# Kernel tuning notes

Hardware: AMD Instinct MI355X
Metric: run time of the kernel (lower is better)

The kernel has to match this reference:

```python
import jax, jax.numpy as jnp
import numpy as np

B, S, D = 2, 2048, 1024
H, HD = 16, 64  # H*HD == D (required by proj layer)
SCALE = D ** -0.5  # NOTE: original scales by full input dim (x.shape[-1]), not head dim


def setup_inputs() -> dict:
    key = jax.random.key(0)
    ks = jax.random.split(key, 7)
    std = D ** -0.5
    x = jax.random.normal(ks[0], (B, S, D), dtype=jnp.float32)
    # per-head projection weights, stacked: [H, D, HD] so x @ Wq[h] == Linear(D->HD)
    Wq = jax.random.normal(ks[1], (H, D, HD), dtype=jnp.float32) * std
    Wk = jax.random.normal(ks[2], (H, D, HD), dtype=jnp.float32) * std
    Wv = jax.random.normal(ks[3], (H, D, HD), dtype=jnp.float32) * std
    # output projection Linear(D, D) with bias
    Wp = jax.random.normal(ks[4], (D, D), dtype=jnp.float32) * std
    bp = jax.random.normal(ks[5], (D,), dtype=jnp.float32) * 0.01
    return {"x": x, "Wq": Wq, "Wk": Wk, "Wv": Wv, "Wp": Wp, "bp": bp}


def reference(x, Wq, Wk, Wv, Wp, bp):
    # All heads see the full x (atsp=False path). Dropout in eval mode (identity).
    q = jnp.einsum('bsd,hde->bhse', x, Wq)  # [B,H,S,HD]
    k = jnp.einsum('bsd,hde->bhse', x, Wk)
    v = jnp.einsum('bsd,hde->bhse', x, Wv)
    scores = jnp.einsum('bhse,bhte->bhst', q, k) * SCALE  # [B,H,S,S]
    causal = jnp.tril(jnp.ones((S, S), dtype=bool))
    scores = jnp.where(causal, scores, -jnp.inf)
    attn = jax.nn.softmax(scores, axis=-1)
    out = jnp.einsum('bhst,bhte->bhse', attn, v)          # [B,H,S,HD]
    # concat heads along last dim in head order: [B,S,H*HD]
    out = out.transpose(0, 2, 1, 3).reshape(B, S, H * HD)
    return out @ Wp.T + bp
```

## Files before the change

### kernel.cpp

```cpp
#include <hip/hip_runtime.h>

typedef __bf16 bf16x8 __attribute__((ext_vector_type(8)));
typedef __bf16 bf16x4 __attribute__((ext_vector_type(4)));
typedef float f32x4 __attribute__((ext_vector_type(4)));
typedef unsigned short u16;
typedef unsigned int u32;

static constexpr int kS = 2048, kD = 1024, kHD = 64;
static constexpr float kQScale = 0.03125f * 1.44269504f;

__device__ __forceinline__ u16 f2bf(float f) {
  union { float f; u32 u; } v; v.f = f;
  u32 r = v.u + 0x7FFFu + ((v.u >> 16) & 1u);
  return (u16)(r >> 16);
}
__device__ __forceinline__ float bf2f(u16 u) {
  union { u32 u; float f; } v; v.u = ((u32)u) << 16;
  return v.f;
}
__device__ __forceinline__ u32 pk2(float a, float b) {
  return (u32)f2bf(a) | ((u32)f2bf(b) << 16);
}
__device__ __forceinline__ f32x4 mfma16(bf16x8 a, bf16x8 b, f32x4 c) {
  return __builtin_amdgcn_mfma_f32_16x16x32_bf16(a, b, c, 0, 0, 0);
}
__device__ __forceinline__ void gld16(u16* lds, const u16* g) {
  __builtin_amdgcn_global_load_lds(
      (const __attribute__((address_space(1))) u32*)g,
      (__attribute__((address_space(3))) u32*)lds, 16, 0, 0);
}

__device__ __forceinline__ bool probe_f32(const u16* __restrict__ xr) {
  int ex = (xr[threadIdx.x] >> 7) & 0xFF;
  int n = __syncthreads_count(ex >= 134);
  return n > 8;
}

union Pack8 { u16 u[8]; uint4 v; };

__global__ void cast_all_kernel(const void* Wq, const void* Wk, const void* Wv,
                                const void* Wp, const void* x,
                                u16* __restrict__ Wt, u16* __restrict__ Wpb,
                                u16* __restrict__ xb) {
  bool f32m = probe_f32((const u16*)x);
  int bid = blockIdx.x;
  int t = threadIdx.x;
  __shared__ float Ts[64][65];
  if (bid < 768) {
    int u = bid >> 4;
    int d0 = (bid & 15) * 64;
    int w = u >> 4, h = u & 15;
    const void* srcv = (w == 0) ? Wq : (w == 1) ? Wk : Wv;
    const float* sf = (const float*)srcv + (size_t)h * kD * kHD;
    const u16*   sb = (const u16*)srcv + (size_t)h * kD * kHD;
    int row = t >> 4;
    int c4 = (t & 15) * 4;
    for (int rr = 0; rr < 64; rr += 16) {
      int r = rr + row;
      if (f32m) {
        float4 v = *(const float4*)&sf[(size_t)(d0 + r) * kHD + c4];
        Ts[r][c4 + 0] = v.x; Ts[r][c4 + 1] = v.y; Ts[r][c4 + 2] = v.z; Ts[r][c4 + 3] = v.w;
      } else {
        const u16* p = &sb[(size_t)(d0 + r) * kHD + c4];
        Ts[r][c4 + 0] = bf2f(p[0]); Ts[r][c4 + 1] = bf2f(p[1]);
        Ts[r][c4 + 2] = bf2f(p[2]); Ts[r][c4 + 3] = bf2f(p[3]);
      }
    }
    __syncthreads();
    for (int rr = 0; rr < 64; rr += 16) {
      int e = rr + row;
      uint2 pk;
      pk.x = pk2(Ts[c4 + 0][e], Ts[c4 + 1][e]);
      pk.y = pk2(Ts[c4 + 2][e], Ts[c4 + 3][e]);
      *(uint2*)&Wt[(size_t)u * (kHD * kD) + (size_t)e * kD + d0 + c4] = pk;
    }
  } else if (bid < 1792) {
    if (!f32m) return;
    int i = ((bid - 768) * 256 + t) * 4;
    float4 v = *(const float4*)((const float*)Wp + i);
    uint2 pk; pk.x = pk2(v.x, v.y); pk.y = pk2(v.z, v.w);
    *(uint2*)&Wpb[i] = pk;
  } else {
    if (!f32m) return;
    size_t i = ((size_t)(bid - 1792) * 256 + t) * 8;
    const float* xf = (const float*)x;
    float4 a = *(const float4*)&xf[i];
    float4 b = *(const float4*)&xf[i + 4];
    Pack8 pk;
    pk.u[0] = f2bf(a.x); pk.u[1] = f2bf(a.y); pk.u[2] = f2bf(a.z); pk.u[3] = f2bf(a.w);
    pk.u[4] = f2bf(b.x); pk.u[5] = f2bf(b.y); pk.u[6] = f2bf(b.z); pk.u[7] = f2bf(b.w);
    *(uint4*)&xb[i] = pk.v;
  }
}

__global__ __launch_bounds__(256) void qkv_gemm_kernel(const u16* __restrict__ xb,
    const u16* __restrict__ Wt, u16* __restrict__ Q, u16* __restrict__ K,
    u16* __restrict__ Vt, const void* __restrict__ x) {
  bool f32m = probe_f32((const u16*)x);
  const u16* xsrc = f32m ? xb : (const u16*)x;
  int m0 = blockIdx.x * 128;
  int n0 = blockIdx.y * 128;
  int w = (int)(blockIdx.y >> 3);
  const u16 *Ap, *Bp; int a0, b0;
  if (w == 2) { Ap = xsrc; a0 = m0; Bp = Wt; b0 = n0; }
  else        { Ap = Wt; a0 = n0; Bp = xsrc; b0 = m0; }
  int t = threadIdx.x;
  int wv = t >> 6, l = t & 63;
  int fr = l & 15, fq = l >> 4;
  int wI = (wv >> 1) * 64, wJ = (wv & 1) * 64;
  __shared__ __align__(16) u16 As[128][64];
  __shared__ __align__(16) u16 Bs[128][64];
  int srow = l >> 3;
  int scol = (((l & 7) ^ srow)) * 8;
  int dcol = (l & 7) * 8;
  int sw = fr & 7;
  f32x4 acc[4][4];
#pragma unroll
  for (int ii = 0; ii < 4; ++ii)
#pragma unroll
    for (int jj = 0; jj < 4; ++jj)
      for (int i = 0; i < 4; ++i) acc[ii][jj][i] = 0.f;

  for (int kb = 0; kb < kD / 64; ++kb) {
    int k0 = kb * 64;
    __syncthreads();
#pragma unroll
    for (int j = 0; j < 4; ++j) {
      int row = (wv * 4 + j) * 8 + srow;
      gld16(&As[row][dcol], &Ap[(size_t)(a0 + row) * kD + k0 + scol]);
      gld16(&Bs[row][dcol], &Bp[(size_t)(b0 + row) * kD + k0 + scol]);
    }
    __syncthreads();
    bf16x8 af[4][2], bg[4][2];
#pragma unroll
    for (int ii = 0; ii < 4; ++ii) {
      af[ii][0] = *(const bf16x8*)&As[wI + ii * 16 + fr][((0 + fq) ^ sw) * 8];
      af[ii][1] = *(const bf16x8*)&As[wI + ii * 16 + fr][((4 + fq) ^ sw) * 8];
    }
#pragma unroll
    for (int jj = 0; jj < 4; ++jj) {
      bg[jj][0] = *(const bf16x8*)&Bs[wJ + jj * 16 + fr][((0 + fq) ^ sw) * 8];
      bg[jj][1] = *(const bf16x8*)&Bs[wJ + jj * 16 + fr][((4 + fq) ^ sw) * 8];
    }
#pragma unroll
    for (int ii = 0; ii < 4; ++ii)
#pragma unroll
      for (int jj = 0; jj < 4; ++jj) {
        acc[ii][jj] = mfma16(af[ii][0], bg[jj][0], acc[ii][jj]);
        acc[ii][jj] = mfma16(af[ii][1], bg[jj][1], acc[ii][jj]);
      }
  }

  if (w == 2) {
    int uh = wv & 1;
    int u = 2 * blockIdx.y + uh;
    int h = u & 15;
#pragma unroll
    for (int jj = 0; jj < 4; ++jj) {
      int e = jj * 16 + fr;
#pragma unroll
      for (int ii = 0; ii < 4; ++ii) {
        int m = m0 + wI + ii * 16 + fq * 4;
        int b = m >> 11, s0 = m & 2047;
        int bh = b * 16 + h;
        *(bf16x4*)&Vt[((size_t)bh * kHD + e) * kS + s0] =
            __builtin_convertvector(acc[ii][jj], bf16x4);
      }
    }
  } else {
    int uh = wv >> 1;
    int u = 2 * blockIdx.y + uh;
    int h = u & 15;
    bool isQ = (w == 0);
    u16* dst = isQ ? Q : K;
#pragma unroll
    for (int jj = 0; jj < 4; ++jj) {
      int m = m0 + wJ + jj * 16 + fr;
      int b = m >> 11, s = m & 2047;
      int bh = b * 16 + h;
      size_t rowb = ((size_t)bh * kS + s) * kHD;
#pragma unroll
      for (int ii = 0; ii < 4; ++ii) {
        int e0 = ii * 16 + fq * 4;
        f32x4 v = acc[ii][jj];
        if (isQ) v *= kQScale;
        *(bf16x4*)&dst[rowb + e0] = __builtin_convertvector(v, bf16x4);
      }
    }
  }
}

__global__ __launch_bounds__(256) void attn_kernel(const u16* __restrict__ Q,
    const u16* __restrict__ K, const u16* __restrict__ Vt, u16* __restrict__ cat) {
  int qb = 31 - (int)(blockIdx.x >> 5);
  int bh = (int)(blockIdx.x & 31);
  int q0 = qb * 64;
  int t = threadIdx.x;
  int wv = t >> 6, l = t & 63;
  int fr = l & 15, fq = l >> 4;
  __shared__ __align__(16) u16 Ks[2][64][64];
  __shared__ __align__(16) u16 Vs[2][64][64];
  __shared__ __align__(16) u16 Ps[4][16][64];
  const u16* Qb = Q + (size_t)bh * kS * kHD;
  const u16* Kb = K + (size_t)bh * kS * kHD;
  const u16* Vb = Vt + (size_t)bh * kHD * kS;

  int qrow = q0 + wv * 16 + fr;
  bf16x8 qf0 = *(const bf16x8*)&Qb[(size_t)qrow * kHD + fq * 8];
  bf16x8 qf1 = *(const bf16x8*)&Qb[(size_t)qrow * kHD + 32 + fq * 8];

  f32x4 O[4];
#pragma unroll
  for (int nt = 0; nt < 4; ++nt) for (int i = 0; i < 4; ++i) O[nt][i] = 0.f;
  float lsum = 0.f;

  int jr = l >> 3;
  int dcol = (l & 7) * 8;
  int scol = ((l & 7) ^ jr) * 8;
  int r0 = wv * 16 + jr;
  int r1 = r0 + 8;
  int sw = fr & 7;

  gld16(&Ks[0][r0][dcol], &Kb[(size_t)r0 * kHD + scol]);
  gld16(&Ks[0][r1][dcol], &Kb[(size_t)r1 * kHD + scol]);
  gld16(&Vs[0][r0][dcol], &Vb[(size_t)r0 * kS + scol]);
  gld16(&Vs[0][r1][dcol], &Vb[(size_t)r1 * kS + scol]);
  __syncthreads();

  int cur = 0;
  for (int tt = 0; tt <= qb; ++tt) {
    int t0 = tt * 64;
    if (tt < qb) {
      int t0n = t0 + 64;
      gld16(&Ks[cur ^ 1][r0][dcol], &Kb[(size_t)(t0n + r0) * kHD + scol]);
      gld16(&Ks[cur ^ 1][r1][dcol], &Kb[(size_t)(t0n + r1) * kHD + scol]);
      gld16(&Vs[cur ^ 1][r0][dcol], &Vb[(size_t)r0 * kS + t0n + scol]);
      gld16(&Vs[cur ^ 1][r1][dcol], &Vb[(size_t)r1 * kS + t0n + scol]);
    }
    f32x4 sc[4];
    __builtin_amdgcn_s_setprio(1);
#pragma unroll
    for (int nt = 0; nt < 4; ++nt) {
      f32x4 z; z[0] = z[1] = z[2] = z[3] = 0.f;
      bf16x8 a0 = *(const bf16x8*)&Ks[cur][nt * 16 + fr][((0 + fq) ^ sw) * 8];
      bf16x8 a1 = *(const bf16x8*)&Ks[cur][nt * 16 + fr][((4 + fq) ^ sw) * 8];
      z = mfma16(a0, qf0, z);
      z = mfma16(a1, qf1, z);
      sc[nt] = z;
    }
    __builtin_amdgcn_s_setprio(0);
    if (tt == qb) {
#pragma unroll
      for (int nt = 0; nt < 4; ++nt)
#pragma unroll
        for (int r = 0; r < 4; ++r)
          if (t0 + nt * 16 + fq * 4 + r > qrow) sc[nt][r] = -__builtin_inff();
    }
#pragma unroll
    for (int nt = 0; nt < 4; ++nt) {
#pragma unroll
      for (int r = 0; r < 4; ++r) {
        float p = exp2f(sc[nt][r]);
        sc[nt][r] = p;
        lsum += p;
      }
      *(bf16x4*)&Ps[wv][fr][(((nt * 2 + (fq >> 1)) ^ sw) * 8) + (fq & 1) * 4] =
          __builtin_convertvector(sc[nt], bf16x4);
    }
    bf16x8 pf0 = *(const bf16x8*)&Ps[wv][fr][(fq ^ sw) * 8];
    bf16x8 pf1 = *(const bf16x8*)&Ps[wv][fr][((4 + fq) ^ sw) * 8];
    __builtin_amdgcn_s_setprio(1);
#pragma unroll
    for (int nt = 0; nt < 4; ++nt) {
      bf16x8 v0 = *(const bf16x8*)&Vs[cur][nt * 16 + fr][((0 + fq) ^ sw) * 8];
      bf16x8 v1 = *(const bf16x8*)&Vs[cur][nt * 16 + fr][((4 + fq) ^ sw) * 8];
      O[nt] = mfma16(v0, pf0, O[nt]);
      O[nt] = mfma16(v1, pf1, O[nt]);
    }
    __builtin_amdgcn_s_setprio(0);
    __syncthreads();
    cur ^= 1;
  }
  lsum += __shfl_xor(lsum, 16, 64);
  lsum += __shfl_xor(lsum, 32, 64);
  float inv = 1.0f / lsum;
  int b = bh >> 4, h = bh & 15;
  size_t rowbase = ((size_t)(b * kS + qrow)) * kD + h * kHD;
#pragma unroll
  for (int nt = 0; nt < 4; ++nt) {
    f32x4 ov = O[nt] * inv;
    *(bf16x4*)&cat[rowbase + nt * 16 + fq * 4] = __builtin_convertvector(ov, bf16x4);
  }
}

__global__ __launch_bounds__(256) void out_gemm_kernel(const u16* __restrict__ cat,
    const u16* __restrict__ Wpb, const void* __restrict__ Wp,
    const void* __restrict__ bp, void* __restrict__ out,
    const void* __restrict__ x) {
  bool f32m = probe_f32((const u16*)x);
  const u16* wsrc = f32m ? Wpb : (const u16*)Wp;
  int m0 = blockIdx.x * 64;
  int n0 = blockIdx.y * 128;
  int t = threadIdx.x;
  int wv = t >> 6, l = t & 63;
  int fr = l & 15, fq = l >> 4;
  int wI = (wv >> 1) * 64, wJ = (wv & 1) * 32;
  __shared__ __align__(16) u16 As[128][64];
  __shared__ __align__(16) u16 Bs[64][64];
  int srow = l >> 3;
  int scol = (((l & 7) ^ srow)) * 8;
  int dcol = (l & 7) * 8;
  int sw = fr & 7;
  f32x4 acc[4][2];
#pragma unroll
  for (int ii = 0; ii < 4; ++ii)
#pragma unroll
    for (int jj = 0; jj < 2; ++jj)
      for (int i = 0; i < 4; ++i) acc[ii][jj][i] = 0.f;

  for (int kb = 0; kb < kD / 64; ++kb) {
    int k0 = kb * 64;
    __syncthreads();
#pragma unroll
    for (int j = 0; j < 4; ++j) {
      int row = j * 32 + wv * 8 + srow;
      gld16(&As[row][dcol], &wsrc[(size_t)(n0 + row) * kD + k0 + scol]);
    }
#pragma unroll
    for (int j = 0; j < 2; ++j) {
      int row = j * 32 + wv * 8 + srow;
      gld16(&Bs[row][dcol], &cat[(size_t)(m0 + row) * kD + k0 + scol]);
    }
    __syncthreads();
    bf16x8 af[4][2], bg[2][2];
#pragma unroll
    for (int ii = 0; ii < 4; ++ii) {
      af[ii][0] = *(const bf16x8*)&As[wI + ii * 16 + fr][((0 + fq) ^ sw) * 8];
      af[ii][1] = *(const bf16x8*)&As[wI + ii * 16 + fr][((4 + fq) ^ sw) * 8];
    }
#pragma unroll
    for (int jj = 0; jj < 2; ++jj) {
      bg[jj][0] = *(const bf16x8*)&Bs[wJ + jj * 16 + fr][((0 + fq) ^ sw) * 8];
      bg[jj][1] = *(const bf16x8*)&Bs[wJ + jj * 16 + fr][((4 + fq) ^ sw) * 8];
    }
#pragma unroll
    for (int ii = 0; ii < 4; ++ii)
#pragma unroll
      for (int jj = 0; jj < 2; ++jj) {
        acc[ii][jj] = mfma16(af[ii][0], bg[jj][0], acc[ii][jj]);
        acc[ii][jj] = mfma16(af[ii][1], bg[jj][1], acc[ii][jj]);
      }
  }
  const float* bpf = (const float*)bp;
  const u16*   bpb = (const u16*)bp;
#pragma unroll
  for (int ii = 0; ii < 4; ++ii) {
    int n = n0 + wI + ii * 16 + fq * 4;
    f32x4 bias;
    if (f32m) bias = *(const f32x4*)&bpf[n];
    else { bias[0] = bf2f(bpb[n]); bias[1] = bf2f(bpb[n + 1]);
           bias[2] = bf2f(bpb[n + 2]); bias[3] = bf2f(bpb[n + 3]); }
#pragma unroll
    for (int jj = 0; jj < 2; ++jj) {
      int m = m0 + wJ + jj * 16 + fr;
      f32x4 v = acc[ii][jj] + bias;
      if (f32m) *(f32x4*)&((float*)out)[(size_t)m * kD + n] = v;
      else      *(bf16x4*)&((u16*)out)[(size_t)m * kD + n] = __builtin_convertvector(v, bf16x4);
    }
  }
}

extern "C" void kernel_launch(void* const* d_in, const int* in_sizes, int n_in,
                              void* d_out, int out_size, void* d_ws, size_t ws_size,
                              hipStream_t stream) {
  const void* x  = d_in[0];
  const void* Wq = d_in[1];
  const void* Wk = d_in[2];
  const void* Wv = d_in[3];
  const void* Wp = d_in[4];
  const void* bp = d_in[5];

  char* ws = (char*)d_ws;
  u16* Wt  = (u16*)(ws + 256);
  u16* Wpb = (u16*)(ws + 256 + 6291456);
  u16* Qp  = (u16*)(ws + 256 + 6291456 + 2097152);
  u16* Kp  = Qp  + (size_t)32 * 2048 * 64;
  u16* Vtp = Kp  + (size_t)32 * 2048 * 64;
  u16* xb  = Vtp + (size_t)32 * 2048 * 64;
  u16* cat = xb;

  cast_all_kernel<<<3840, 256, 0, stream>>>(Wq, Wk, Wv, Wp, x, Wt, Wpb, xb);
  qkv_gemm_kernel<<<dim3(32, 24), 256, 0, stream>>>(xb, Wt, Qp, Kp, Vtp, x);
  attn_kernel<<<1024, 256, 0, stream>>>(Qp, Kp, Vtp, cat);
  out_gemm_kernel<<<dim3(64, 8), 256, 0, stream>>>(cat, Wpb, Wp, bp, d_out, x);
}
```

Baseline: 173.1 us.

## Split long causal attention query blocks across two workgroups with combine pass

Query blocks in the upper half of the causal range are split into two workgroups, each covering half of the key tiles. Partial unnormalized outputs and row sums go to fp32 workspace, and a new combine kernel sums them and normalizes. A schedule table orders blocks to balance load across CUs, which targets the tail imbalance of the causal triangle. In exchange it adds an extra kernel launch and fp32 partial traffic. The partials skip max rescaling, which relies on there being no running max in this kernel.

```diff
diff --git a/kernel.cpp b/kernel.cpp
--- a/kernel.cpp
+++ b/kernel.cpp
@@ -190,10 +190,40 @@
   }
 }
 
+static __device__ const signed char kQtab[48] = {
+  15,31,30,31,
+  14,29,28,30,29,
+  13,27,26,28,27,
+  12,25,24,26,25,
+  11,23,22,24,23,
+  10,21,20,22,21,
+   9,19,18,20,19,
+   8,17,16,18,17,
+   7,16,
+   6,5,4,3,2,1,0};
+static __device__ const signed char kPtab[48] = {
+  2,0,0,1,
+  2,0,0,1,1,
+  2,0,0,1,1,
+  2,0,0,1,1,
+  2,0,0,1,1,
+  2,0,0,1,1,
+  2,0,0,1,1,
+  2,0,0,1,1,
+  2,1,
+  2,2,2,2,2,2,2};
+
 __global__ __launch_bounds__(256) void attn_kernel(const u16* __restrict__ Q,
-    const u16* __restrict__ K, const u16* __restrict__ Vt, u16* __restrict__ cat) {
-  int qb = 31 - (int)(blockIdx.x >> 5);
+    const u16* __restrict__ K, const u16* __restrict__ Vt, u16* __restrict__ cat,
+    float* __restrict__ Po, float* __restrict__ Pl, int split) {
   int bh = (int)(blockIdx.x & 31);
+  int c  = (int)(blockIdx.x >> 5);
+  int qb, part;
+  if (split) { qb = kQtab[c]; part = kPtab[c]; }
+  else       { qb = 31 - c;   part = 2; }
+  int h0 = (qb + 2) >> 1;
+  int tbeg = (part == 1) ? h0 : 0;
+  int tend = (part == 0) ? h0 - 1 : qb;
   int q0 = qb * 64;
   int t = threadIdx.x;
   int wv = t >> 6, l = t & 63;
@@ -221,16 +251,19 @@
   int r1 = r0 + 8;
   int sw = fr & 7;
 
-  gld16(&Ks[0][r0][dcol], &Kb[(size_t)r0 * kHD + scol]);
-  gld16(&Ks[0][r1][dcol], &Kb[(size_t)r1 * kHD + scol]);
-  gld16(&Vs[0][r0][dcol], &Vb[(size_t)r0 * kS + scol]);
-  gld16(&Vs[0][r1][dcol], &Vb[(size_t)r1 * kS + scol]);
+  {
+    int tb = tbeg * 64;
+    gld16(&Ks[0][r0][dcol], &Kb[(size_t)(tb + r0) * kHD + scol]);
+    gld16(&Ks[0][r1][dcol], &Kb[(size_t)(tb + r1) * kHD + scol]);
+    gld16(&Vs[0][r0][dcol], &Vb[(size_t)r0 * kS + tb + scol]);
+    gld16(&Vs[0][r1][dcol], &Vb[(size_t)r1 * kS + tb + scol]);
+  }
   __syncthreads();
 
   int cur = 0;
-  for (int tt = 0; tt <= qb; ++tt) {
+  for (int tt = tbeg; tt <= tend; ++tt) {
     int t0 = tt * 64;
-    if (tt < qb) {
+    if (tt < tend) {
       int t0n = t0 + 64;
       gld16(&Ks[cur ^ 1][r0][dcol], &Kb[(size_t)(t0n + r0) * kHD + scol]);
       gld16(&Ks[cur ^ 1][r1][dcol], &Kb[(size_t)(t0n + r1) * kHD + scol]);
@@ -283,13 +316,45 @@
   }
   lsum += __shfl_xor(lsum, 16, 64);
   lsum += __shfl_xor(lsum, 32, 64);
-  float inv = 1.0f / lsum;
+  if (part == 2) {
+    float inv = 1.0f / lsum;
+    int b = bh >> 4, h = bh & 15;
+    size_t rowbase = ((size_t)(b * kS + qrow)) * kD + h * kHD;
+#pragma unroll
+    for (int nt = 0; nt < 4; ++nt) {
+      f32x4 ov = O[nt] * inv;
+      *(bf16x4*)&cat[rowbase + nt * 16 + fq * 4] = __builtin_convertvector(ov, bf16x4);
+    }
+  } else {
+    int slot = ((bh << 4) + (qb - 16)) * 2 + part;
+    float* Pb = Po + (size_t)slot * 4096 + (wv * 16 + fr) * 64;
+    if (fq == 0) Pl[slot * 64 + wv * 16 + fr] = lsum;
+#pragma unroll
+    for (int nt = 0; nt < 4; ++nt)
+      *(f32x4*)&Pb[nt * 16 + fq * 4] = O[nt];
+  }
+}
+
+__global__ __launch_bounds__(256) void attn_combine_kernel(
+    const float* __restrict__ Po, const float* __restrict__ Pl,
+    u16* __restrict__ cat) {
+  int bh = (int)(blockIdx.x >> 4);
+  int lvl = (int)(blockIdx.x & 15);
+  int t = threadIdx.x;
+  int slot = ((bh << 4) + lvl) * 2;
   int b = bh >> 4, h = bh & 15;
-  size_t rowbase = ((size_t)(b * kS + qrow)) * kD + h * kHD;
-#pragma unroll
-  for (int nt = 0; nt < 4; ++nt) {
-    f32x4 ov = O[nt] * inv;
-    *(bf16x4*)&cat[rowbase + nt * 16 + fq * 4] = __builtin_convertvector(ov, bf16x4);
+  int e0 = (t & 15) * 4;
+  for (int qq = 0; qq < 64; qq += 16) {
+    int q = qq + (t >> 4);
+    const float* A = Po + (size_t)slot * 4096 + q * 64 + e0;
+    float l = Pl[slot * 64 + q] + Pl[(slot + 1) * 64 + q];
+    float inv = 1.0f / l;
+    f32x4 a = *(const f32x4*)A;
+    f32x4 bv = *(const f32x4*)(A + 4096);
+    f32x4 v = (a + bv) * inv;
+    int qrow = (lvl + 16) * 64 + q;
+    *(bf16x4*)&cat[((size_t)(b * kS + qrow)) * kD + h * kHD + e0] =
+        __builtin_convertvector(v, bf16x4);
   }
 }
 
@@ -388,9 +453,17 @@
   u16* Vtp = Kp  + (size_t)32 * 2048 * 64;
   u16* xb  = Vtp + (size_t)32 * 2048 * 64;
   u16* cat = xb;
+  size_t poOff = 256 + 6291456 + 2097152 + (size_t)4 * 8388608;
+  size_t plOff = poOff + (size_t)32 * 16 * 2 * 4096 * 4;
+  size_t needWs = plOff + (size_t)32 * 16 * 2 * 64 * 4;
+  int split = (ws_size >= needWs) ? 1 : 0;
+  float* Po = (float*)(ws + poOff);
+  float* Pl = (float*)(ws + plOff);
 
   cast_all_kernel<<<3840, 256, 0, stream>>>(Wq, Wk, Wv, Wp, x, Wt, Wpb, xb);
   qkv_gemm_kernel<<<dim3(32, 24), 256, 0, stream>>>(xb, Wt, Qp, Kp, Vtp, x);
-  attn_kernel<<<1024, 256, 0, stream>>>(Qp, Kp, Vtp, cat);
+  attn_kernel<<<split ? 1536 : 1024, 256, 0, stream>>>(Qp, Kp, Vtp, cat, Po, Pl, split);
+  if (split)
+    attn_combine_kernel<<<512, 256, 0, stream>>>(Po, Pl, cat);
   out_gemm_kernel<<<dim3(64, 8), 256, 0, stream>>>(cat, Wpb, Wp, bp, d_out, x);
 }
```

After: 179.3 us. 1.04x slower.

## Permute K rows on load so P stays in registers for PV MFMA

Applied to the files above, without the earlier changes.

Loads K tile rows in a permuted order so that the score MFMA output fragment layout directly matches the B-operand layout needed by the PV MFMA. This removes the per-wave LDS round trip for P (the store, the reload and the Ps buffer) and adjusts the causal mask indices to the permuted key positions. It cuts LDS traffic and shared memory use, and relies on the permutation being applied consistently to K, the mask and the V operand ordering.

```diff
diff --git a/kernel.cpp b/kernel.cpp
--- a/kernel.cpp
+++ b/kernel.cpp
@@ -200,7 +200,6 @@
   int fr = l & 15, fq = l >> 4;
   __shared__ __align__(16) u16 Ks[2][64][64];
   __shared__ __align__(16) u16 Vs[2][64][64];
-  __shared__ __align__(16) u16 Ps[4][16][64];
   const u16* Qb = Q + (size_t)bh * kS * kHD;
   const u16* Kb = K + (size_t)bh * kS * kHD;
   const u16* Vb = Vt + (size_t)bh * kHD * kS;
@@ -219,10 +218,12 @@
   int scol = ((l & 7) ^ jr) * 8;
   int r0 = wv * 16 + jr;
   int r1 = r0 + 8;
+  int gk0 = 8 * ((r0 >> 2) & 3) + 4 * ((r0 >> 4) & 1) + 32 * (r0 >> 5) + (r0 & 3);
+  int gk1 = 8 * ((r1 >> 2) & 3) + 4 * ((r1 >> 4) & 1) + 32 * (r1 >> 5) + (r1 & 3);
   int sw = fr & 7;
 
-  gld16(&Ks[0][r0][dcol], &Kb[(size_t)r0 * kHD + scol]);
-  gld16(&Ks[0][r1][dcol], &Kb[(size_t)r1 * kHD + scol]);
+  gld16(&Ks[0][r0][dcol], &Kb[(size_t)gk0 * kHD + scol]);
+  gld16(&Ks[0][r1][dcol], &Kb[(size_t)gk1 * kHD + scol]);
   gld16(&Vs[0][r0][dcol], &Vb[(size_t)r0 * kS + scol]);
   gld16(&Vs[0][r1][dcol], &Vb[(size_t)r1 * kS + scol]);
   __syncthreads();
@@ -232,8 +233,8 @@
     int t0 = tt * 64;
     if (tt < qb) {
       int t0n = t0 + 64;
-      gld16(&Ks[cur ^ 1][r0][dcol], &Kb[(size_t)(t0n + r0) * kHD + scol]);
-      gld16(&Ks[cur ^ 1][r1][dcol], &Kb[(size_t)(t0n + r1) * kHD + scol]);
+      gld16(&Ks[cur ^ 1][r0][dcol], &Kb[(size_t)(t0n + gk0) * kHD + scol]);
+      gld16(&Ks[cur ^ 1][r1][dcol], &Kb[(size_t)(t0n + gk1) * kHD + scol]);
       gld16(&Vs[cur ^ 1][r0][dcol], &Vb[(size_t)r0 * kS + t0n + scol]);
       gld16(&Vs[cur ^ 1][r1][dcol], &Vb[(size_t)r1 * kS + t0n + scol]);
     }
@@ -254,28 +255,29 @@
       for (int nt = 0; nt < 4; ++nt)
 #pragma unroll
         for (int r = 0; r < 4; ++r)
-          if (t0 + nt * 16 + fq * 4 + r > qrow) sc[nt][r] = -__builtin_inff();
-    }
-#pragma unroll
-    for (int nt = 0; nt < 4; ++nt) {
+          if (t0 + 8 * fq + 4 * (nt & 1) + 32 * (nt >> 1) + r > qrow)
+            sc[nt][r] = -__builtin_inff();
+    }
+#pragma unroll
+    for (int nt = 0; nt < 4; ++nt)
 #pragma unroll
       for (int r = 0; r < 4; ++r) {
         float p = exp2f(sc[nt][r]);
         sc[nt][r] = p;
         lsum += p;
       }
-      *(bf16x4*)&Ps[wv][fr][(((nt * 2 + (fq >> 1)) ^ sw) * 8) + (fq & 1) * 4] =
-          __builtin_convertvector(sc[nt], bf16x4);
-    }
-    bf16x8 pf0 = *(const bf16x8*)&Ps[wv][fr][(fq ^ sw) * 8];
-    bf16x8 pf1 = *(const bf16x8*)&Ps[wv][fr][((4 + fq) ^ sw) * 8];
+    union PB { bf16x4 h[2]; bf16x8 v; } pb0, pb1;
+    pb0.h[0] = __builtin_convertvector(sc[0], bf16x4);
+    pb0.h[1] = __builtin_convertvector(sc[1], bf16x4);
+    pb1.h[0] = __builtin_convertvector(sc[2], bf16x4);
+    pb1.h[1] = __builtin_convertvector(sc[3], bf16x4);
     __builtin_amdgcn_s_setprio(1);
 #pragma unroll
     for (int nt = 0; nt < 4; ++nt) {
       bf16x8 v0 = *(const bf16x8*)&Vs[cur][nt * 16 + fr][((0 + fq) ^ sw) * 8];
       bf16x8 v1 = *(const bf16x8*)&Vs[cur][nt * 16 + fr][((4 + fq) ^ sw) * 8];
-      O[nt] = mfma16(v0, pf0, O[nt]);
-      O[nt] = mfma16(v1, pf1, O[nt]);
+      O[nt] = mfma16(v0, pb0.v, O[nt]);
+      O[nt] = mfma16(v1, pb1.v, O[nt]);
     }
     __builtin_amdgcn_s_setprio(0);
     __syncthreads();
```

Result: no change. 172.7 us (-0.3%).
